# Kernel optimization log

Hardware: AMD Instinct MI355X
Metric: run time of the kernel (lower is better)

## Reference

```python
import jax, jax.numpy as jnp
import numpy as np

B, N, M, NUM_CLASSES = 16, 2048, 2048, 40


def setup_inputs() -> dict:
    key = jax.random.key(0)
    k1, k2, k3, k4 = jax.random.split(key, 4)
    reg = jax.random.normal(k1, (B, N, 3), dtype=jnp.float32)
    point1 = jax.random.normal(k2, (B, M, 3), dtype=jnp.float32)
    # pred is expected to be log-probabilities (output of log_softmax)
    pred = jax.nn.log_softmax(jax.random.normal(k3, (B, NUM_CLASSES), dtype=jnp.float32), axis=-1)
    target = jax.random.randint(k4, (B,), 0, NUM_CLASSES, dtype=jnp.int64)
    return {"reg": reg, "point1": point1, "pred": pred, "target": target}


def _chamfer(x, y):
    # x: [B, N, 3], y: [B, M, 3]
    x2 = jnp.sum(x * x, axis=-1)                      # [B, N]
    y2 = jnp.sum(y * y, axis=-1)                      # [B, M]
    xy = jnp.einsum('bnd,bmd->bnm', x, y)             # [B, N, M]
    d = x2[:, :, None] + y2[:, None, :] - 2.0 * xy    # [B, N, M]
    dist1 = jnp.min(d, axis=2)                        # [B, N] nearest y for each x
    dist2 = jnp.min(d, axis=1)                        # [B, M] nearest x for each y
    return dist1, dist2


def reference(reg, point1, pred, target):
    # NLL loss with mean reduction: -mean(pred[b, target[b]])
    nll = -jnp.mean(jnp.take_along_axis(pred, target[:, None].astype(jnp.int32), axis=1))
    dist1, dist2 = _chamfer(reg, point1)
    reg_loss = jnp.mean(jnp.mean(dist1, axis=1) + jnp.mean(dist2, axis=1))
    return nll + reg_loss
```

## Files before the change

kernel.cpp:

```cpp
#include <hip/hip_runtime.h>
#include <hip/hip_bf16.h>


#define NPTS 2048
#define BATCH 16
#define NCLS 40
#define KQ 8
#define MB 256
#define SEGLEN 32
#define NBLOCKS 2048
#define TABLE 65536

__global__ __launch_bounds__(256, 4) void chamfer_kernel(const float* __restrict__ reg,
                                                         const float* __restrict__ pt,
                                                         unsigned int* __restrict__ tab) {
    int bid = blockIdx.x;
    int dir = bid >> 10;
    int rem = bid & 1023;
    int b = rem >> 6;
    int rem2 = rem & 63;
    int nch = rem2 >> 3;
    int mq = rem2 & 7;

    const float* __restrict__ X = dir ? pt : reg;
    const float* __restrict__ Y = dir ? reg : pt;

    __shared__ float4 sy[8][SEGLEN + 1];
    __shared__ float4 sq[256];

    int tid = threadIdx.x;

    {
        const float* Yb = Y + (size_t)b * (NPTS * 3) + (size_t)(mq * MB) * 3;
        float y0 = Yb[tid * 3], y1 = Yb[tid * 3 + 1], y2 = Yb[tid * 3 + 2];
        sy[tid >> 5][tid & 31] = make_float4(y0, y1, y2, fmaf(y0, y0, fmaf(y1, y1, y2 * y2)));
        const float* Xb = X + (size_t)b * (NPTS * 3) + (size_t)(nch * 256) * 3;
        float x0 = Xb[tid * 3], x1 = Xb[tid * 3 + 1], x2 = Xb[tid * 3 + 2];
        sq[tid] = make_float4(-2.f * x0, -2.f * x1, -2.f * x2,
                              fmaf(x0, x0, fmaf(x1, x1, x2 * x2)));
    }
    __syncthreads();

    int lane = tid & 63;
    int wave = tid >> 6;
    int g = lane & 7;
    int s = lane >> 3;

    float ax[KQ], ay[KQ], az[KQ], mn[KQ];
#pragma unroll
    for (int i = 0; i < KQ; ++i) {
        float4 q = sq[wave * 64 + g * KQ + i];
        ax[i] = q.x; ay[i] = q.y; az[i] = q.z;
        mn[i] = 3.0e38f;
    }

    const float4* ysp = &sy[s][0];
#pragma unroll 4
    for (int m = 0; m < SEGLEN; ++m) {
        float4 y = ysp[m];
#pragma unroll
        for (int i = 0; i < KQ; ++i) {
            float d = fmaf(ax[i], y.x, fmaf(ay[i], y.y, fmaf(az[i], y.z, y.w)));
            mn[i] = fminf(mn[i], d);
        }
    }

#pragma unroll
    for (int i = 0; i < KQ; ++i) {
        mn[i] = fminf(mn[i], __shfl_xor(mn[i], 8));
        mn[i] = fminf(mn[i], __shfl_xor(mn[i], 16));
        mn[i] = fminf(mn[i], __shfl_xor(mn[i], 32));
    }

    if (s == 0) {
        unsigned int* t = tab + dir * 32768 + b * NPTS + nch * 256 + wave * 64 + g * KQ;
#pragma unroll
        for (int i = 0; i < KQ; ++i) {
            float v = fmaxf(sq[wave * 64 + g * KQ + i].w + mn[i], 0.f);
            atomicMin(&t[i], __float_as_uint(v));
        }
    }
}

__global__ __launch_bounds__(1024) void finalize_kernel(const unsigned int* __restrict__ tab,
                                                        const float* __restrict__ pred,
                                                        const int* __restrict__ target,
                                                        float* __restrict__ out) {
    __shared__ float wsum[16];
    __shared__ float nll_s;
    int tid = threadIdx.x;

    if (tid < 64) {
        float nv = (tid < BATCH) ? pred[tid * NCLS + target[tid]] : 0.f;
        for (int off = 8; off > 0; off >>= 1) nv += __shfl_down(nv, off);
        if (tid == 0) nll_s = nv;
    }

    const uint4* t4 = (const uint4*)tab;
    float v = 0.f;
#pragma unroll
    for (int k = 0; k < 16; ++k) {
        uint4 u = t4[k * 1024 + tid];
        v += __uint_as_float(u.x) + __uint_as_float(u.y) +
             __uint_as_float(u.z) + __uint_as_float(u.w);
    }
    for (int off = 32; off > 0; off >>= 1) v += __shfl_down(v, off);
    int lane = tid & 63, wid = tid >> 6;
    if (lane == 0) wsum[wid] = v;
    __syncthreads();
    if (tid == 0) {
        float s = 0.f;
#pragma unroll
        for (int w = 0; w < 16; ++w) s += wsum[w];
        out[0] = s * (1.0f / (BATCH * NPTS)) - nll_s * (1.0f / BATCH);
    }
}

extern "C" void kernel_launch(void* const* d_in, const int* in_sizes, int n_in,
                              void* d_out, int out_size, void* d_ws, size_t ws_size,
                              hipStream_t stream) {
    const float* reg    = (const float*)d_in[0];
    const float* point1 = (const float*)d_in[1];
    const float* pred   = (const float*)d_in[2];
    const int*   target = (const int*)d_in[3];
    float* out = (float*)d_out;
    unsigned int* tab = (unsigned int*)d_ws;

    chamfer_kernel<<<NBLOCKS, 256, 0, stream>>>(reg, point1, tab);
    finalize_kernel<<<1, 1024, 0, stream>>>(tab, pred, target, out);
}
```

Before: 78.87 us.

## Give each block full Y range and replace atomicMin table with block partial sums

After: 74.64 us. -5.4%, faster.

```diff
diff --git a/kernel.cpp b/kernel.cpp
--- a/kernel.cpp
+++ b/kernel.cpp
@@ -6,57 +6,59 @@
 #define BATCH 16
 #define NCLS 40
 #define KQ 8
-#define MB 256
-#define SEGLEN 32
-#define NBLOCKS 2048
-#define TABLE 65536
+#define NBLOCKS 512
 
-__global__ __launch_bounds__(256, 4) void chamfer_kernel(const float* __restrict__ reg,
-                                                         const float* __restrict__ pt,
-                                                         unsigned int* __restrict__ tab) {
+__global__ __launch_bounds__(512) void chamfer_kernel(const float* __restrict__ reg,
+                                                      const float* __restrict__ pt,
+                                                      float* __restrict__ partial) {
     int bid = blockIdx.x;
-    int dir = bid >> 10;
-    int rem = bid & 1023;
-    int b = rem >> 6;
-    int rem2 = rem & 63;
-    int nch = rem2 >> 3;
-    int mq = rem2 & 7;
+    int dir = bid >> 8;
+    int rem = bid & 255;
+    int b = rem >> 4;
+    int nch = rem & 15;
 
     const float* __restrict__ X = dir ? pt : reg;
     const float* __restrict__ Y = dir ? reg : pt;
 
-    __shared__ float4 sy[8][SEGLEN + 1];
-    __shared__ float4 sq[256];
+    __shared__ float4 sy[32][65];
+    __shared__ float4 sq[16][9];
+    __shared__ float  sm[128][5];
+    __shared__ float  red[2];
 
     int tid = threadIdx.x;
 
-    {
-        const float* Yb = Y + (size_t)b * (NPTS * 3) + (size_t)(mq * MB) * 3;
-        float y0 = Yb[tid * 3], y1 = Yb[tid * 3 + 1], y2 = Yb[tid * 3 + 2];
-        sy[tid >> 5][tid & 31] = make_float4(y0, y1, y2, fmaf(y0, y0, fmaf(y1, y1, y2 * y2)));
-        const float* Xb = X + (size_t)b * (NPTS * 3) + (size_t)(nch * 256) * 3;
+    const float* Yb = Y + (size_t)b * (NPTS * 3);
+    for (int p = tid; p < NPTS; p += 512) {
+        float y0 = Yb[p * 3], y1 = Yb[p * 3 + 1], y2 = Yb[p * 3 + 2];
+        sy[p >> 6][p & 63] = make_float4(y0, y1, y2, fmaf(y0, y0, fmaf(y1, y1, y2 * y2)));
+    }
+    if (tid < 128) {
+        const float* Xb = X + (size_t)b * (NPTS * 3) + (size_t)(nch * 128) * 3;
         float x0 = Xb[tid * 3], x1 = Xb[tid * 3 + 1], x2 = Xb[tid * 3 + 2];
-        sq[tid] = make_float4(-2.f * x0, -2.f * x1, -2.f * x2,
-                              fmaf(x0, x0, fmaf(x1, x1, x2 * x2)));
+        sq[tid >> 3][tid & 7] = make_float4(-2.f * x0, -2.f * x1, -2.f * x2,
+                                            fmaf(x0, x0, fmaf(x1, x1, x2 * x2)));
     }
     __syncthreads();
 
     int lane = tid & 63;
     int wave = tid >> 6;
+    int qh = wave >> 1;
+    int qw = wave & 1;
     int g = lane & 7;
     int s = lane >> 3;
 
     float ax[KQ], ay[KQ], az[KQ], mn[KQ];
 #pragma unroll
     for (int i = 0; i < KQ; ++i) {
-        float4 q = sq[wave * 64 + g * KQ + i];
-        ax[i] = q.x; ay[i] = q.y; az[i] = q.z;
+        int q = qw * 64 + g * 8 + i;
+        float4 qv = sq[q >> 3][q & 7];
+        ax[i] = qv.x; ay[i] = qv.y; az[i] = qv.z;
         mn[i] = 3.0e38f;
     }
 
-    const float4* ysp = &sy[s][0];
+    const float4* ysp = &sy[qh * 8 + s][0];
 #pragma unroll 4
-    for (int m = 0; m < SEGLEN; ++m) {
+    for (int m = 0; m < 64; ++m) {
         float4 y = ysp[m];
 #pragma unroll
         for (int i = 0; i < KQ; ++i) {
@@ -71,22 +73,28 @@
         mn[i] = fminf(mn[i], __shfl_xor(mn[i], 16));
         mn[i] = fminf(mn[i], __shfl_xor(mn[i], 32));
     }
+    if (s == 0) {
+#pragma unroll
+        for (int i = 0; i < KQ; ++i) sm[qw * 64 + g * 8 + i][qh] = mn[i];
+    }
+    __syncthreads();
 
-    if (s == 0) {
-        unsigned int* t = tab + dir * 32768 + b * NPTS + nch * 256 + wave * 64 + g * KQ;
-#pragma unroll
-        for (int i = 0; i < KQ; ++i) {
-            float v = fmaxf(sq[wave * 64 + g * KQ + i].w + mn[i], 0.f);
-            atomicMin(&t[i], __float_as_uint(v));
-        }
+    float v = 0.f;
+    if (tid < 128) {
+        float m0 = fminf(fminf(sm[tid][0], sm[tid][1]), fminf(sm[tid][2], sm[tid][3]));
+        v = fmaxf(sq[tid >> 3][tid & 7].w + m0, 0.f);
     }
+    for (int off = 32; off > 0; off >>= 1) v += __shfl_down(v, off);
+    if (tid < 128 && lane == 0) red[wave] = v;
+    __syncthreads();
+    if (tid == 0) partial[bid] = red[0] + red[1];
 }
 
-__global__ __launch_bounds__(1024) void finalize_kernel(const unsigned int* __restrict__ tab,
-                                                        const float* __restrict__ pred,
-                                                        const int* __restrict__ target,
-                                                        float* __restrict__ out) {
-    __shared__ float wsum[16];
+__global__ __launch_bounds__(512) void finalize_kernel(const float* __restrict__ partial,
+                                                       const float* __restrict__ pred,
+                                                       const int* __restrict__ target,
+                                                       float* __restrict__ out) {
+    __shared__ float wsum[8];
     __shared__ float nll_s;
     int tid = threadIdx.x;
 
@@ -96,22 +104,14 @@
         if (tid == 0) nll_s = nv;
     }
 
-    const uint4* t4 = (const uint4*)tab;
-    float v = 0.f;
-#pragma unroll
-    for (int k = 0; k < 16; ++k) {
-        uint4 u = t4[k * 1024 + tid];
-        v += __uint_as_float(u.x) + __uint_as_float(u.y) +
-             __uint_as_float(u.z) + __uint_as_float(u.w);
-    }
+    float v = partial[tid];
     for (int off = 32; off > 0; off >>= 1) v += __shfl_down(v, off);
-    int lane = tid & 63, wid = tid >> 6;
-    if (lane == 0) wsum[wid] = v;
+    if ((tid & 63) == 0) wsum[tid >> 6] = v;
     __syncthreads();
     if (tid == 0) {
         float s = 0.f;
 #pragma unroll
-        for (int w = 0; w < 16; ++w) s += wsum[w];
+        for (int w = 0; w < 8; ++w) s += wsum[w];
         out[0] = s * (1.0f / (BATCH * NPTS)) - nll_s * (1.0f / BATCH);
     }
 }
@@ -124,8 +124,8 @@
     const float* pred   = (const float*)d_in[2];
     const int*   target = (const int*)d_in[3];
     float* out = (float*)d_out;
-    unsigned int* tab = (unsigned int*)d_ws;
+    float* partial = (float*)d_ws;
 
-    chamfer_kernel<<<NBLOCKS, 256, 0, stream>>>(reg, point1, tab);
-    finalize_kernel<<<1, 1024, 0, stream>>>(tab, pred, target, out);
+    chamfer_kernel<<<NBLOCKS, 512, 0, stream>>>(reg, point1, partial);
+    finalize_kernel<<<1, 512, 0, stream>>>(partial, pred, target, out);
 }
```
